# Optimization experiments

Measured on AMD Instinct MI355X. Metric: run time of the kernel, lower is better.

## Reference

```python
import jax, jax.numpy as jnp
import numpy as np

N = 100000      # nodes
E = 1600000     # edges (avg degree 16)
IN, H, OUT = 128, 128, 64


def setup_inputs() -> dict:
    key = jax.random.key(0)
    ks = jax.random.split(key, 6)
    x = jax.random.normal(ks[0], (N, IN), dtype=jnp.float32)
    edge_index = jax.random.randint(ks[1], (2, E), 0, N, dtype=jnp.int64)
    # normalize=False => adj_t values hold precomputed GCN norm weights
    edge_weight = jax.random.uniform(ks[2], (E,), dtype=jnp.float32)

    def glorot(k, fi, fo):
        lim = np.sqrt(6.0 / (fi + fo)).astype(np.float32)
        return jax.random.uniform(k, (fi, fo), jnp.float32, -lim, lim)

    W1, b1 = glorot(ks[3], IN, H), jnp.zeros((H,), jnp.float32)
    W2, b2 = glorot(ks[4], H, H), jnp.zeros((H,), jnp.float32)
    W3, b3 = glorot(ks[5], H, OUT), jnp.zeros((OUT,), jnp.float32)
    return {"x": x, "edge_index": edge_index, "edge_weight": edge_weight,
            "W1": W1, "b1": b1, "W2": W2, "b2": b2, "W3": W3, "b3": b3}


def _gcn_conv(x, W, b, src, dst, w):
    # GCNConv(normalize=False): linear transform then weighted scatter-sum (adj_t @ h)
    h = x @ W                                    # [N, F_out]
    msg = h[src] * w[:, None]                    # gather + weight, [E, F_out]
    agg = jax.ops.segment_sum(msg, dst, num_segments=N)
    return agg + b


def reference(x, edge_index, edge_weight, W1, b1, W2, b2, W3, b3):
    src, dst = edge_index[0], edge_index[1]
    h = jax.nn.relu(_gcn_conv(x, W1, b1, src, dst, edge_weight))
    # dropout is identity at inference (training=False)
    h = jax.nn.relu(_gcn_conv(h, W2, b2, src, dst, edge_weight))
    return _gcn_conv(h, W3, b3, src, dst, edge_weight)
```

## Files before the change

### kernel.cpp

```cpp
#include <hip/hip_runtime.h>


typedef __attribute__((ext_vector_type(8))) short short8;
typedef __attribute__((ext_vector_type(4))) float f32x4;

__device__ __forceinline__ unsigned short f2bf(float f) {
  union { float f; unsigned u; } v; v.f = f;
  unsigned r = v.u + 0x7fffu + ((v.u >> 16) & 1u);
  return (unsigned short)(r >> 16);
}
__device__ __forceinline__ float bf2f(unsigned short h) {
  union { unsigned u; float f; } v; v.u = (unsigned)h << 16;
  return v.f;
}

constexpr int ABLK = 256;
constexpr int BINSHIFT = 8;
constexpr int MAXBINS = 512;

__global__ __launch_bounds__(256) void binhist_kernel(
    const int* __restrict__ dst, int* __restrict__ G, int E, int nbins,
    int chunk) {
  __shared__ int h[MAXBINS];
  for (int i = threadIdx.x; i < nbins; i += 256) h[i] = 0;
  __syncthreads();
  const int base = blockIdx.x * chunk;
  const int end = min(base + chunk, E);
  for (int i = base + threadIdx.x; i < end; i += 256)
    atomicAdd(&h[__builtin_nontemporal_load(dst + i) >> BINSHIFT], 1);
  __syncthreads();
  for (int i = threadIdx.x; i < nbins; i += 256)
    G[i * ABLK + blockIdx.x] = h[i];
}

__global__ __launch_bounds__(256) void scan_local_kernel(
    int* __restrict__ G, int* __restrict__ binTot) {
  __shared__ int sc[256];
  const int b = blockIdx.x;
  const int v = G[b * ABLK + threadIdx.x];
  sc[threadIdx.x] = v;
  __syncthreads();
  for (int off = 1; off < 256; off <<= 1) {
    const int mine = sc[threadIdx.x];
    const int add = (threadIdx.x >= off) ? sc[threadIdx.x - off] : 0;
    __syncthreads();
    sc[threadIdx.x] = mine + add;
    __syncthreads();
  }
  G[b * ABLK + threadIdx.x] = sc[threadIdx.x] - v;
  if (threadIdx.x == 255) binTot[b] = sc[255];
}

__global__ __launch_bounds__(256) void scan_bins_kernel(
    const int* __restrict__ binTot, int* __restrict__ binBase, int nbins,
    int E) {
  __shared__ int sc[512];
  sc[threadIdx.x] = (threadIdx.x < nbins) ? binTot[threadIdx.x] : 0;
  sc[threadIdx.x + 256] =
      (threadIdx.x + 256 < nbins) ? binTot[threadIdx.x + 256] : 0;
  for (int d = 1; d < 512; d <<= 1) {
    __syncthreads();
    const int idx = (threadIdx.x + 1) * (d << 1) - 1;
    if (idx < 512) sc[idx] += sc[idx - d];
  }
  __syncthreads();
  if (threadIdx.x == 0) sc[511] = 0;
  for (int d = 256; d >= 1; d >>= 1) {
    __syncthreads();
    const int idx = (threadIdx.x + 1) * (d << 1) - 1;
    if (idx < 512) {
      const int tmp = sc[idx - d];
      sc[idx - d] = sc[idx];
      sc[idx] += tmp;
    }
  }
  __syncthreads();
  if (threadIdx.x < nbins) binBase[threadIdx.x] = sc[threadIdx.x];
  if (threadIdx.x + 256 < nbins) binBase[threadIdx.x + 256] = sc[threadIdx.x + 256];
  if (threadIdx.x == 0) binBase[nbins] = E;
}

__global__ __launch_bounds__(256) void binscatter_kernel(
    const int* __restrict__ src, const int* __restrict__ dst,
    const float* __restrict__ ew, const int* __restrict__ G,
    const int* __restrict__ binBase, int* __restrict__ bdst,
    int2* __restrict__ bsw, int E, int nbins, int chunk) {
  __shared__ int cur[MAXBINS];
  for (int i = threadIdx.x; i < nbins; i += 256)
    cur[i] = binBase[i] + G[i * ABLK + blockIdx.x];
  __syncthreads();
  const int base = blockIdx.x * chunk;
  const int end = min(base + chunk, E);
  for (int i = base + threadIdx.x; i < end; i += 256) {
    const int d = __builtin_nontemporal_load(dst + i);
    const int s = __builtin_nontemporal_load(src + i);
    const float w = __builtin_nontemporal_load(ew + i);
    const int p = atomicAdd(&cur[d >> BINSHIFT], 1);
    bdst[p] = d;
    bsw[p] = make_int2(s, __float_as_int(w));
  }
}

__global__ __launch_bounds__(256) void csrbuild_kernel(
    const int* __restrict__ bdst, const int2* __restrict__ bsw,
    const int* __restrict__ binBase, int* __restrict__ rowptr,
    int2* __restrict__ csr, int N, int E, int nbins) {
  __shared__ int deg[256];
  __shared__ int sc[256];
  const int b = blockIdx.x;
  const int node0 = b << BINSHIFT;
  const int nnode = min(256, N - node0);
  const int beg = binBase[b];
  const int end = binBase[b + 1];

  deg[threadIdx.x] = 0;
  __syncthreads();
  for (int i = beg + threadIdx.x; i < end; i += 256)
    atomicAdd(&deg[bdst[i] & 255], 1);
  __syncthreads();

  const int s = deg[threadIdx.x];
  sc[threadIdx.x] = s;
  __syncthreads();
  for (int off = 1; off < 256; off <<= 1) {
    const int mine = sc[threadIdx.x];
    const int add = (threadIdx.x >= off) ? sc[threadIdx.x - off] : 0;
    __syncthreads();
    sc[threadIdx.x] = mine + add;
    __syncthreads();
  }
  const int rp = beg + sc[threadIdx.x] - s;
  if (threadIdx.x < nnode) rowptr[node0 + threadIdx.x] = rp;
  deg[threadIdx.x] = rp;
  __syncthreads();
  for (int i = beg + threadIdx.x; i < end; i += 256) {
    const int p = atomicAdd(&deg[bdst[i] & 255], 1);
    csr[p] = bsw[i];
  }
  if (b == 0 && threadIdx.x == 0) rowptr[N] = E;
}

__global__ __launch_bounds__(256) void prep_w_kernel(
    const float* __restrict__ W1, const float* __restrict__ W2,
    const float* __restrict__ W3, unsigned short* __restrict__ WT1,
    unsigned short* __restrict__ WT2, unsigned short* __restrict__ WT3) {
  const int id = blockIdx.x * 256 + threadIdx.x;
  const float* W;
  unsigned short* WT;
  int NC, idx;
  if (id < 16384) { W = W1; WT = WT1; NC = 128; idx = id; }
  else if (id < 32768) { W = W2; WT = WT2; NC = 128; idx = id - 16384; }
  else if (id < 40960) { W = W3; WT = WT3; NC = 64; idx = id - 32768; }
  else return;
  const int k = idx / NC, n = idx % NC;
  *(unsigned short*)((char*)WT + n * 256 + ((2 * k) ^ ((n & 7) << 4))) =
      f2bf(W[idx]);
}

template <int NC, bool IN_F32>
__global__ __launch_bounds__(256) void gemm_mfma_kernel(
    const void* __restrict__ in, const unsigned short* __restrict__ WT,
    unsigned short* __restrict__ outp, int nrows) {
  constexpr int NT = NC / 16;
  __shared__ unsigned short Wlds[NC * 128];
  {
    const float4* wsrc = (const float4*)WT;
    float4* wdst = (float4*)Wlds;
    for (int i = threadIdx.x; i < NC * 256 / 16; i += 256) wdst[i] = wsrc[i];
  }
  __syncthreads();

  const int lane = threadIdx.x & 63;
  const int wave = threadIdx.x >> 6;
  const int nl = lane & 15;
  const int kl = (lane >> 4) * 8;
  const int rb = blockIdx.x * 64 + wave * 16;
  const int ra = min(rb + nl, nrows - 1);
  const int swz = (nl & 7) << 4;
  const char* wbase = (const char*)Wlds + nl * 256;

  f32x4 acc[NT] = {};

#pragma unroll
  for (int k0 = 0; k0 < 128; k0 += 32) {
    short8 a;
    if (IN_F32) {
      const float* xp = (const float*)in + (size_t)ra * 128 + k0 + kl;
      const float4 x0 = *(const float4*)xp;
      const float4 x1 = *(const float4*)(xp + 4);
      a[0] = (short)f2bf(x0.x); a[1] = (short)f2bf(x0.y);
      a[2] = (short)f2bf(x0.z); a[3] = (short)f2bf(x0.w);
      a[4] = (short)f2bf(x1.x); a[5] = (short)f2bf(x1.y);
      a[6] = (short)f2bf(x1.z); a[7] = (short)f2bf(x1.w);
    } else {
      a = *(const short8*)((const unsigned short*)in + (size_t)ra * 128 + k0 + kl);
    }
    const int koff = (2 * (k0 + kl)) ^ swz;
#pragma unroll
    for (int ct = 0; ct < NT; ++ct) {
      const short8 b = *(const short8*)(wbase + ct * 4096 + koff);
      acc[ct] = __builtin_amdgcn_mfma_f32_16x16x32_bf16(a, b, acc[ct], 0, 0, 0);
    }
  }

  const int r0 = rb + (lane >> 4) * 4;
#pragma unroll
  for (int ct = 0; ct < NT; ++ct) {
#pragma unroll
    for (int j = 0; j < 4; ++j) {
      const int r = r0 + j;
      if (r < nrows) outp[(size_t)r * NC + ct * 16 + nl] = f2bf(acc[ct][j]);
    }
  }
}

__device__ __forceinline__ void edge_unpack(long c, int& s, float& w) {
  s = (int)c;
  w = __int_as_float((int)(c >> 32));
}

template <bool BF16OUT>
__global__ __launch_bounds__(256) void gather128_kernel(
    const unsigned short* __restrict__ t, const long* __restrict__ csr,
    const int* __restrict__ rowptr, const float* __restrict__ bias,
    void* __restrict__ outp, int n) {
  const int lane = threadIdx.x & 63;
  const int node = blockIdx.x * 4 + (threadIdx.x >> 6);
  if (node >= n) return;
  const int beg = __builtin_amdgcn_readfirstlane(rowptr[node]);
  const int end = __builtin_amdgcn_readfirstlane(rowptr[node + 1]);

  float2 a0 = *(const float2*)&bias[lane * 2];
  float2 a1 = {0.f, 0.f}, a2 = {0.f, 0.f}, a3 = {0.f, 0.f};
  int e = beg;
  for (; e + 4 <= end; e += 4) {
    int s0, s1, s2, s3;
    float w0, w1, w2, w3;
    edge_unpack(__builtin_nontemporal_load(csr + e), s0, w0);
    edge_unpack(__builtin_nontemporal_load(csr + e + 1), s1, w1);
    edge_unpack(__builtin_nontemporal_load(csr + e + 2), s2, w2);
    edge_unpack(__builtin_nontemporal_load(csr + e + 3), s3, w3);
    const unsigned v0 = *(const unsigned*)&t[(size_t)s0 * 128 + lane * 2];
    const unsigned v1 = *(const unsigned*)&t[(size_t)s1 * 128 + lane * 2];
    const unsigned v2 = *(const unsigned*)&t[(size_t)s2 * 128 + lane * 2];
    const unsigned v3 = *(const unsigned*)&t[(size_t)s3 * 128 + lane * 2];
    a0.x = fmaf(bf2f((unsigned short)v0), w0, a0.x);
    a0.y = fmaf(bf2f((unsigned short)(v0 >> 16)), w0, a0.y);
    a1.x = fmaf(bf2f((unsigned short)v1), w1, a1.x);
    a1.y = fmaf(bf2f((unsigned short)(v1 >> 16)), w1, a1.y);
    a2.x = fmaf(bf2f((unsigned short)v2), w2, a2.x);
    a2.y = fmaf(bf2f((unsigned short)(v2 >> 16)), w2, a2.y);
    a3.x = fmaf(bf2f((unsigned short)v3), w3, a3.x);
    a3.y = fmaf(bf2f((unsigned short)(v3 >> 16)), w3, a3.y);
  }
  for (; e < end; ++e) {
    int s0; float w0;
    edge_unpack(__builtin_nontemporal_load(csr + e), s0, w0);
    const unsigned v0 = *(const unsigned*)&t[(size_t)s0 * 128 + lane * 2];
    a0.x = fmaf(bf2f((unsigned short)v0), w0, a0.x);
    a0.y = fmaf(bf2f((unsigned short)(v0 >> 16)), w0, a0.y);
  }
  a0.x += a1.x + a2.x + a3.x;
  a0.y += a1.y + a2.y + a3.y;
  if (BF16OUT) {
    a0.x = fmaxf(a0.x, 0.f);
    a0.y = fmaxf(a0.y, 0.f);
    const unsigned pk = (unsigned)f2bf(a0.x) | ((unsigned)f2bf(a0.y) << 16);
    *(unsigned*)((unsigned short*)outp + (size_t)node * 128 + lane * 2) = pk;
  } else {
    *(float2*)((float*)outp + (size_t)node * 128 + lane * 2) = a0;
  }
}

__global__ __launch_bounds__(256) void gather64_kernel(
    const unsigned short* __restrict__ t, const long* __restrict__ csr,
    const int* __restrict__ rowptr, const float* __restrict__ bias,
    float* __restrict__ outp, int n) {
  const int lane = threadIdx.x & 63;
  const int node = blockIdx.x * 4 + (threadIdx.x >> 6);
  if (node >= n) return;
  const int beg = __builtin_amdgcn_readfirstlane(rowptr[node]);
  const int end = __builtin_amdgcn_readfirstlane(rowptr[node + 1]);
  float a0 = bias[lane], a1 = 0.f, a2 = 0.f, a3 = 0.f;
  int e = beg;
  for (; e + 4 <= end; e += 4) {
    int s0, s1, s2, s3;
    float w0, w1, w2, w3;
    edge_unpack(__builtin_nontemporal_load(csr + e), s0, w0);
    edge_unpack(__builtin_nontemporal_load(csr + e + 1), s1, w1);
    edge_unpack(__builtin_nontemporal_load(csr + e + 2), s2, w2);
    edge_unpack(__builtin_nontemporal_load(csr + e + 3), s3, w3);
    a0 = fmaf(bf2f(t[(size_t)s0 * 64 + lane]), w0, a0);
    a1 = fmaf(bf2f(t[(size_t)s1 * 64 + lane]), w1, a1);
    a2 = fmaf(bf2f(t[(size_t)s2 * 64 + lane]), w2, a2);
    a3 = fmaf(bf2f(t[(size_t)s3 * 64 + lane]), w3, a3);
  }
  for (; e < end; ++e) {
    int s0; float w0;
    edge_unpack(__builtin_nontemporal_load(csr + e), s0, w0);
    a0 = fmaf(bf2f(t[(size_t)s0 * 64 + lane]), w0, a0);
  }
  outp[(size_t)node * 64 + lane] = a0 + a1 + a2 + a3;
}

extern "C" void kernel_launch(void* const* d_in, const int* in_sizes, int n_in,
                              void* d_out, int out_size, void* d_ws, size_t ws_size,
                              hipStream_t stream) {
  const float* x  = (const float*)d_in[0];
  const int*   ei = (const int*)d_in[1];
  const float* ew = (const float*)d_in[2];
  const float* W1 = (const float*)d_in[3];
  const float* b1 = (const float*)d_in[4];
  const float* W2 = (const float*)d_in[5];
  const float* b2 = (const float*)d_in[6];
  const float* W3 = (const float*)d_in[7];
  const float* b3 = (const float*)d_in[8];

  const int E = in_sizes[2];
  const int N = in_sizes[0] / 128;
  const int* src = ei;
  const int* dst = ei + E;

  const int nbins = (N + 255) >> BINSHIFT;
  const int chunk = (E + ABLK - 1) / ABLK;

  unsigned short* WT1 = (unsigned short*)d_ws;
  unsigned short* WT2 = WT1 + 16384;
  unsigned short* WT3 = WT2 + 16384;
  unsigned short* t = WT3 + 8192;
  unsigned short* g = t + (size_t)N * 128;
  int2* csr = (int2*)(g + (size_t)N * 128);
  int* rowptr = (int*)(csr + E);
  int* G = rowptr + (N + 1);
  int* binTot = G + nbins * ABLK;
  int* binBase = binTot + nbins;
  int2* bsw = (int2*)g;
  int* bdst = (int*)(bsw + E);

  const int gemm_blocks = (N + 63) / 64;
  const int gather_blocks = (N + 3) / 4;

  prep_w_kernel<<<160, 256, 0, stream>>>(W1, W2, W3, WT1, WT2, WT3);
  binhist_kernel<<<ABLK, 256, 0, stream>>>(dst, G, E, nbins, chunk);
  scan_local_kernel<<<nbins, 256, 0, stream>>>(G, binTot);
  scan_bins_kernel<<<1, 256, 0, stream>>>(binTot, binBase, nbins, E);
  binscatter_kernel<<<ABLK, 256, 0, stream>>>(src, dst, ew, G, binBase, bdst,
                                              bsw, E, nbins, chunk);
  csrbuild_kernel<<<nbins, 256, 0, stream>>>(bdst, bsw, binBase, rowptr, csr,
                                             N, E, nbins);

  gemm_mfma_kernel<128, true><<<gemm_blocks, 256, 0, stream>>>(x, WT1, t, N);
  gather128_kernel<true><<<gather_blocks, 256, 0, stream>>>(
      t, (const long*)csr, rowptr, b1, g, N);

  gemm_mfma_kernel<128, false><<<gemm_blocks, 256, 0, stream>>>(g, WT2, t, N);
  gather128_kernel<true><<<gather_blocks, 256, 0, stream>>>(
      t, (const long*)csr, rowptr, b2, g, N);

  gemm_mfma_kernel<64, false><<<gemm_blocks, 256, 0, stream>>>(g, WT3, t, N);
  gather64_kernel<<<gather_blocks, 256, 0, stream>>>(
      t, (const long*)csr, rowptr, b3, (float*)d_out, N);
}
```

Baseline: 301.0 us.

## Pack dst into src bits, stage bins in LDS, multi-node-per-wave gathers

```diff
diff --git a/kernel.cpp b/kernel.cpp
--- a/kernel.cpp
+++ b/kernel.cpp
@@ -17,6 +17,8 @@
 constexpr int ABLK = 256;
 constexpr int BINSHIFT = 8;
 constexpr int MAXBINS = 512;
+constexpr int SRCBITS = 17;
+constexpr int SRCMASK = (1 << SRCBITS) - 1;
 
 __global__ __launch_bounds__(256) void binhist_kernel(
     const int* __restrict__ dst, int* __restrict__ G, int E, int nbins,
@@ -83,8 +85,8 @@
 __global__ __launch_bounds__(256) void binscatter_kernel(
     const int* __restrict__ src, const int* __restrict__ dst,
     const float* __restrict__ ew, const int* __restrict__ G,
-    const int* __restrict__ binBase, int* __restrict__ bdst,
-    int2* __restrict__ bsw, int E, int nbins, int chunk) {
+    const int* __restrict__ binBase, int2* __restrict__ bsw, int E, int nbins,
+    int chunk) {
   __shared__ int cur[MAXBINS];
   for (int i = threadIdx.x; i < nbins; i += 256)
     cur[i] = binBase[i] + G[i * ABLK + blockIdx.x];
@@ -96,27 +98,31 @@
     const int s = __builtin_nontemporal_load(src + i);
     const float w = __builtin_nontemporal_load(ew + i);
     const int p = atomicAdd(&cur[d >> BINSHIFT], 1);
-    bdst[p] = d;
-    bsw[p] = make_int2(s, __float_as_int(w));
+    bsw[p] = make_int2(s | ((d & 255) << SRCBITS), __float_as_int(w));
   }
 }
 
 __global__ __launch_bounds__(256) void csrbuild_kernel(
-    const int* __restrict__ bdst, const int2* __restrict__ bsw,
-    const int* __restrict__ binBase, int* __restrict__ rowptr,
-    int2* __restrict__ csr, int N, int E, int nbins) {
+    const long* __restrict__ bsw, const int* __restrict__ binBase,
+    int* __restrict__ rowptr, int2* __restrict__ csr, int N, int E,
+    int nbins) {
+  constexpr int CAP = 6144;
+  __shared__ long stage[CAP];
   __shared__ int deg[256];
   __shared__ int sc[256];
   const int b = blockIdx.x;
   const int node0 = b << BINSHIFT;
-  const int nnode = min(256, N - node0);
   const int beg = binBase[b];
-  const int end = binBase[b + 1];
+  const int cnt = binBase[b + 1] - beg;
+  const bool fit = (cnt <= CAP);
 
   deg[threadIdx.x] = 0;
   __syncthreads();
-  for (int i = beg + threadIdx.x; i < end; i += 256)
-    atomicAdd(&deg[bdst[i] & 255], 1);
+  for (int i = threadIdx.x; i < cnt; i += 256) {
+    const long c = __builtin_nontemporal_load(bsw + beg + i);
+    if (fit) stage[i] = c;
+    atomicAdd(&deg[((int)c >> SRCBITS) & 255], 1);
+  }
   __syncthreads();
 
   const int s = deg[threadIdx.x];
@@ -130,12 +136,14 @@
     __syncthreads();
   }
   const int rp = beg + sc[threadIdx.x] - s;
-  if (threadIdx.x < nnode) rowptr[node0 + threadIdx.x] = rp;
+  if (node0 + threadIdx.x < N) rowptr[node0 + threadIdx.x] = rp;
   deg[threadIdx.x] = rp;
   __syncthreads();
-  for (int i = beg + threadIdx.x; i < end; i += 256) {
-    const int p = atomicAdd(&deg[bdst[i] & 255], 1);
-    csr[p] = bsw[i];
+  for (int i = threadIdx.x; i < cnt; i += 256) {
+    const long c = fit ? stage[i] : bsw[beg + i];
+    const int lo = (int)c;
+    const int p = atomicAdd(&deg[(lo >> SRCBITS) & 255], 1);
+    csr[p] = make_int2(lo & SRCMASK, (int)(c >> 32));
   }
   if (b == 0 && threadIdx.x == 0) rowptr[N] = E;
 }
@@ -214,9 +222,15 @@
   }
 }
 
-__device__ __forceinline__ void edge_unpack(long c, int& s, float& w) {
-  s = (int)c;
-  w = __int_as_float((int)(c >> 32));
+__device__ __forceinline__ void acc_edge128(const unsigned short* t, long c,
+                                            int hl, float4& a) {
+  const int s = (int)c;
+  const float w = __int_as_float((int)(c >> 32));
+  const uint2 v = *(const uint2*)&t[(size_t)s * 128 + hl * 4];
+  a.x = fmaf(bf2f((unsigned short)v.x), w, a.x);
+  a.y = fmaf(bf2f((unsigned short)(v.x >> 16)), w, a.y);
+  a.z = fmaf(bf2f((unsigned short)v.y), w, a.z);
+  a.w = fmaf(bf2f((unsigned short)(v.y >> 16)), w, a.w);
 }
 
 template <bool BF16OUT>
@@ -224,83 +238,86 @@
     const unsigned short* __restrict__ t, const long* __restrict__ csr,
     const int* __restrict__ rowptr, const float* __restrict__ bias,
     void* __restrict__ outp, int n) {
-  const int lane = threadIdx.x & 63;
-  const int node = blockIdx.x * 4 + (threadIdx.x >> 6);
+  const int wave = threadIdx.x >> 6;
+  const int half = (threadIdx.x >> 5) & 1;
+  const int hl = threadIdx.x & 31;
+  const int node = blockIdx.x * 8 + wave * 2 + half;
   if (node >= n) return;
-  const int beg = __builtin_amdgcn_readfirstlane(rowptr[node]);
-  const int end = __builtin_amdgcn_readfirstlane(rowptr[node + 1]);
-
-  float2 a0 = *(const float2*)&bias[lane * 2];
-  float2 a1 = {0.f, 0.f}, a2 = {0.f, 0.f}, a3 = {0.f, 0.f};
-  int e = beg;
+  int e = rowptr[node];
+  const int end = rowptr[node + 1];
+
+  float4 a0 = *(const float4*)&bias[hl * 4];
+  float4 a1 = {0, 0, 0, 0}, a2 = {0, 0, 0, 0}, a3 = {0, 0, 0, 0};
   for (; e + 4 <= end; e += 4) {
-    int s0, s1, s2, s3;
-    float w0, w1, w2, w3;
-    edge_unpack(__builtin_nontemporal_load(csr + e), s0, w0);
-    edge_unpack(__builtin_nontemporal_load(csr + e + 1), s1, w1);
-    edge_unpack(__builtin_nontemporal_load(csr + e + 2), s2, w2);
-    edge_unpack(__builtin_nontemporal_load(csr + e + 3), s3, w3);
-    const unsigned v0 = *(const unsigned*)&t[(size_t)s0 * 128 + lane * 2];
-    const unsigned v1 = *(const unsigned*)&t[(size_t)s1 * 128 + lane * 2];
-    const unsigned v2 = *(const unsigned*)&t[(size_t)s2 * 128 + lane * 2];
-    const unsigned v3 = *(const unsigned*)&t[(size_t)s3 * 128 + lane * 2];
-    a0.x = fmaf(bf2f((unsigned short)v0), w0, a0.x);
-    a0.y = fmaf(bf2f((unsigned short)(v0 >> 16)), w0, a0.y);
-    a1.x = fmaf(bf2f((unsigned short)v1), w1, a1.x);
-    a1.y = fmaf(bf2f((unsigned short)(v1 >> 16)), w1, a1.y);
-    a2.x = fmaf(bf2f((unsigned short)v2), w2, a2.x);
-    a2.y = fmaf(bf2f((unsigned short)(v2 >> 16)), w2, a2.y);
-    a3.x = fmaf(bf2f((unsigned short)v3), w3, a3.x);
-    a3.y = fmaf(bf2f((unsigned short)(v3 >> 16)), w3, a3.y);
-  }
-  for (; e < end; ++e) {
-    int s0; float w0;
-    edge_unpack(__builtin_nontemporal_load(csr + e), s0, w0);
-    const unsigned v0 = *(const unsigned*)&t[(size_t)s0 * 128 + lane * 2];
-    a0.x = fmaf(bf2f((unsigned short)v0), w0, a0.x);
-    a0.y = fmaf(bf2f((unsigned short)(v0 >> 16)), w0, a0.y);
-  }
+    const long c0 = __builtin_nontemporal_load(csr + e);
+    const long c1 = __builtin_nontemporal_load(csr + e + 1);
+    const long c2 = __builtin_nontemporal_load(csr + e + 2);
+    const long c3 = __builtin_nontemporal_load(csr + e + 3);
+    acc_edge128(t, c0, hl, a0);
+    acc_edge128(t, c1, hl, a1);
+    acc_edge128(t, c2, hl, a2);
+    acc_edge128(t, c3, hl, a3);
+  }
+  for (; e < end; ++e)
+    acc_edge128(t, __builtin_nontemporal_load(csr + e), hl, a0);
   a0.x += a1.x + a2.x + a3.x;
   a0.y += a1.y + a2.y + a3.y;
+  a0.z += a1.z + a2.z + a3.z;
+  a0.w += a1.w + a2.w + a3.w;
   if (BF16OUT) {
-    a0.x = fmaxf(a0.x, 0.f);
-    a0.y = fmaxf(a0.y, 0.f);
-    const unsigned pk = (unsigned)f2bf(a0.x) | ((unsigned)f2bf(a0.y) << 16);
-    *(unsigned*)((unsigned short*)outp + (size_t)node * 128 + lane * 2) = pk;
+    a0.x = fmaxf(a0.x, 0.f); a0.y = fmaxf(a0.y, 0.f);
+    a0.z = fmaxf(a0.z, 0.f); a0.w = fmaxf(a0.w, 0.f);
+    uint2 pk;
+    pk.x = (unsigned)f2bf(a0.x) | ((unsigned)f2bf(a0.y) << 16);
+    pk.y = (unsigned)f2bf(a0.z) | ((unsigned)f2bf(a0.w) << 16);
+    *(uint2*)((unsigned short*)outp + (size_t)node * 128 + hl * 4) = pk;
   } else {
-    *(float2*)((float*)outp + (size_t)node * 128 + lane * 2) = a0;
-  }
+    *(float4*)((float*)outp + (size_t)node * 128 + hl * 4) = a0;
+  }
+}
+
+__device__ __forceinline__ void acc_edge64(const unsigned short* t, long c,
+                                           int ql, float4& a) {
+  const int s = (int)c;
+  const float w = __int_as_float((int)(c >> 32));
+  const uint2 v = *(const uint2*)&t[(size_t)s * 64 + ql * 4];
+  a.x = fmaf(bf2f((unsigned short)v.x), w, a.x);
+  a.y = fmaf(bf2f((unsigned short)(v.x >> 16)), w, a.y);
+  a.z = fmaf(bf2f((unsigned short)v.y), w, a.z);
+  a.w = fmaf(bf2f((unsigned short)(v.y >> 16)), w, a.w);
 }
 
 __global__ __launch_bounds__(256) void gather64_kernel(
     const unsigned short* __restrict__ t, const long* __restrict__ csr,
     const int* __restrict__ rowptr, const float* __restrict__ bias,
     float* __restrict__ outp, int n) {
-  const int lane = threadIdx.x & 63;
-  const int node = blockIdx.x * 4 + (threadIdx.x >> 6);
+  const int wave = threadIdx.x >> 6;
+  const int q = (threadIdx.x >> 4) & 3;
+  const int ql = threadIdx.x & 15;
+  const int node = blockIdx.x * 16 + wave * 4 + q;
   if (node >= n) return;
-  const int beg = __builtin_amdgcn_readfirstlane(rowptr[node]);
-  const int end = __builtin_amdgcn_readfirstlane(rowptr[node + 1]);
-  float a0 = bias[lane], a1 = 0.f, a2 = 0.f, a3 = 0.f;
-  int e = beg;
+  int e = rowptr[node];
+  const int end = rowptr[node + 1];
+
+  float4 a0 = *(const float4*)&bias[ql * 4];
+  float4 a1 = {0, 0, 0, 0}, a2 = {0, 0, 0, 0}, a3 = {0, 0, 0, 0};
   for (; e + 4 <= end; e += 4) {
-    int s0, s1, s2, s3;
-    float w0, w1, w2, w3;
-    edge_unpack(__builtin_nontemporal_load(csr + e), s0, w0);
-    edge_unpack(__builtin_nontemporal_load(csr + e + 1), s1, w1);
-    edge_unpack(__builtin_nontemporal_load(csr + e + 2), s2, w2);
-    edge_unpack(__builtin_nontemporal_load(csr + e + 3), s3, w3);
-    a0 = fmaf(bf2f(t[(size_t)s0 * 64 + lane]), w0, a0);
-    a1 = fmaf(bf2f(t[(size_t)s1 * 64 + lane]), w1, a1);
-    a2 = fmaf(bf2f(t[(size_t)s2 * 64 + lane]), w2, a2);
-    a3 = fmaf(bf2f(t[(size_t)s3 * 64 + lane]), w3, a3);
-  }
-  for (; e < end; ++e) {
-    int s0; float w0;
-    edge_unpack(__builtin_nontemporal_load(csr + e), s0, w0);
-    a0 = fmaf(bf2f(t[(size_t)s0 * 64 + lane]), w0, a0);
-  }
-  outp[(size_t)node * 64 + lane] = a0 + a1 + a2 + a3;
+    const long c0 = __builtin_nontemporal_load(csr + e);
+    const long c1 = __builtin_nontemporal_load(csr + e + 1);
+    const long c2 = __builtin_nontemporal_load(csr + e + 2);
+    const long c3 = __builtin_nontemporal_load(csr + e + 3);
+    acc_edge64(t, c0, ql, a0);
+    acc_edge64(t, c1, ql, a1);
+    acc_edge64(t, c2, ql, a2);
+    acc_edge64(t, c3, ql, a3);
+  }
+  for (; e < end; ++e)
+    acc_edge64(t, __builtin_nontemporal_load(csr + e), ql, a0);
+  a0.x += a1.x + a2.x + a3.x;
+  a0.y += a1.y + a2.y + a3.y;
+  a0.z += a1.z + a2.z + a3.z;
+  a0.w += a1.w + a2.w + a3.w;
+  *(float4*)&outp[(size_t)node * 64 + ql * 4] = a0;
 }
 
 extern "C" void kernel_launch(void* const* d_in, const int* in_sizes, int n_in,
@@ -335,29 +352,29 @@
   int* binTot = G + nbins * ABLK;
   int* binBase = binTot + nbins;
   int2* bsw = (int2*)g;
-  int* bdst = (int*)(bsw + E);
 
   const int gemm_blocks = (N + 63) / 64;
-  const int gather_blocks = (N + 3) / 4;
+  const int g128_blocks = (N + 7) / 8;
+  const int g64_blocks = (N + 15) / 16;
 
   prep_w_kernel<<<160, 256, 0, stream>>>(W1, W2, W3, WT1, WT2, WT3);
   binhist_kernel<<<ABLK, 256, 0, stream>>>(dst, G, E, nbins, chunk);
   scan_local_kernel<<<nbins, 256, 0, stream>>>(G, binTot);
   scan_bins_kernel<<<1, 256, 0, stream>>>(binTot, binBase, nbins, E);
-  binscatter_kernel<<<ABLK, 256, 0, stream>>>(src, dst, ew, G, binBase, bdst,
-                                              bsw, E, nbins, chunk);
-  csrbuild_kernel<<<nbins, 256, 0, stream>>>(bdst, bsw, binBase, rowptr, csr,
-                                             N, E, nbins);
+  binscatter_kernel<<<ABLK, 256, 0, stream>>>(src, dst, ew, G, binBase, bsw,
+                                              E, nbins, chunk);
+  csrbuild_kernel<<<nbins, 256, 0, stream>>>((const long*)bsw, binBase,
+                                             rowptr, csr, N, E, nbins);
 
   gemm_mfma_kernel<128, true><<<gemm_blocks, 256, 0, stream>>>(x, WT1, t, N);
-  gather128_kernel<true><<<gather_blocks, 256, 0, stream>>>(
+  gather128_kernel<true><<<g128_blocks, 256, 0, stream>>>(
       t, (const long*)csr, rowptr, b1, g, N);
 
   gemm_mfma_kernel<128, false><<<gemm_blocks, 256, 0, stream>>>(g, WT2, t, N);
-  gather128_kernel<true><<<gather_blocks, 256, 0, stream>>>(
+  gather128_kernel<true><<<g128_blocks, 256, 0, stream>>>(
       t, (const long*)csr, rowptr, b2, g, N);
 
   gemm_mfma_kernel<64, false><<<gemm_blocks, 256, 0, stream>>>(g, WT3, t, N);
-  gather64_kernel<<<gather_blocks, 256, 0, stream>>>(
+  gather64_kernel<<<g64_blocks, 256, 0, stream>>>(
       t, (const long*)csr, rowptr, b3, (float*)d_out, N);
 }
```

After: 294.1 us. 2.3% less time.
